# Optimization experiments

Hardware: AMD Instinct MI355X
Metric: run time of the kernel (lower is better)

## Reference

```python
import jax, jax.numpy as jnp
import numpy as np

CODEBOOK_SIZE = 1024
CODEBOOK_DIM = 64
COMMITMENT_WEIGHT = 0.25
DECAY = 0.99
EPS = 1e-5


def setup_inputs() -> dict:
    key = jax.random.key(0)
    k1, k2, k3 = jax.random.split(key, 3)
    B, D, T = 32, CODEBOOK_DIM, 4096
    z = jax.random.normal(k1, (B, D, T), dtype=jnp.float32)
    embedding = jax.random.normal(k2, (CODEBOOK_SIZE, CODEBOOK_DIM), dtype=jnp.float32)
    cluster_size = jnp.zeros((CODEBOOK_SIZE,), dtype=jnp.float32)
    embed_avg = jax.random.normal(k3, (CODEBOOK_SIZE, CODEBOOK_DIM), dtype=jnp.float32)
    return {"z": z, "embedding": embedding, "cluster_size": cluster_size, "embed_avg": embed_avg}


def reference(z, embedding, cluster_size, embed_avg):
    # z: [B, D, T]; embedding/embed_avg: [K, D]; cluster_size: [K]
    B, D, T = z.shape
    K = embedding.shape[0]
    z_flat = jnp.transpose(z, (0, 2, 1)).reshape(-1, D)  # [N, D], N = B*T

    # squared-euclidean distances via expansion (matches torch cdist expansion)
    dist = (
        jnp.sum(z_flat * z_flat, axis=1, keepdims=True)
        + jnp.sum(embedding * embedding, axis=1)
        - 2.0 * (z_flat @ embedding.T)
    )  # [N, K]
    indices = jnp.argmin(dist, axis=1)  # [N] int

    # EMA updates (training path). one_hot.sum(0) -> segment count; one_hot.T @ z_flat -> segment sum
    counts = jax.ops.segment_sum(jnp.ones(z_flat.shape[0], dtype=z_flat.dtype), indices, num_segments=K)
    new_cluster_size = cluster_size * DECAY + (1.0 - DECAY) * counts
    embed_sum = jax.ops.segment_sum(z_flat, indices, num_segments=K)  # [K, D]
    new_embed_avg = embed_avg * DECAY + (1.0 - DECAY) * embed_sum
    n = jnp.sum(new_cluster_size)
    smoothed = (new_cluster_size + EPS) / (n + K * EPS) * n  # Laplace smoothing
    new_embedding = new_embed_avg / smoothed[:, None]  # [K, D]

    # quantize with the *updated* codebook (as in the torch in-place update)
    z_q_flat = new_embedding[indices]  # [N, D] gather
    loss = COMMITMENT_WEIGHT * jnp.mean((z_flat - jax.lax.stop_gradient(z_q_flat)) ** 2)
    # straight-through estimator
    z_q_flat = z_flat + jax.lax.stop_gradient(z_q_flat - z_flat)
    z_q = jnp.transpose(z_q_flat.reshape(B, T, D), (0, 2, 1))  # [B, D, T]
    return z_q, loss, indices.reshape(B, T)
```

## Files before the change

kernel.cpp:

```cpp
#include <hip/hip_runtime.h>

#define N_PTS 131072
#define TD 4096
#define DD 64
#define KK 1024
#define MARGIN_TH 2e-3f
#define BPAD 72

typedef short bf16x8 __attribute__((ext_vector_type(8)));
typedef float f32x4  __attribute__((ext_vector_type(4)));

__device__ inline unsigned short f2bf(float f) {
    unsigned u = __float_as_uint(f);
    unsigned r = u + 0x7FFFu + ((u >> 16) & 1u);
    return (unsigned short)(r >> 16);
}
__device__ inline float bf2f(unsigned short h) {
    return __uint_as_float(((unsigned)h) << 16);
}

__global__ __launch_bounds__(256) void vq_prep(const float* __restrict__ z,
                                               unsigned short* __restrict__ zh,
                                               unsigned short* __restrict__ zl)
{
    __shared__ float tile[64][65];
    const int tid = threadIdx.x;
    const int b = blockIdx.x >> 6;
    const int t0 = (blockIdx.x & 63) * 64;

    const int d = tid >> 2, tq = tid & 3;
#pragma unroll
    for (int it = 0; it < 4; ++it) {
        const int tt = tq * 16 + it * 4;
        const float4 v = *(const float4*)(z + ((size_t)b * DD + d) * TD + t0 + tt);
        tile[d][tt] = v.x; tile[d][tt + 1] = v.y; tile[d][tt + 2] = v.z; tile[d][tt + 3] = v.w;
    }
    __syncthreads();

    const int p = tid >> 2, dg = tid & 3;
    bf16x8 h0, h1, l0, l1;
#pragma unroll
    for (int j = 0; j < 8; ++j) {
        const float v0 = tile[dg * 16 + j][p];
        const unsigned short a = f2bf(v0);
        h0[j] = (short)a; l0[j] = (short)f2bf(v0 - bf2f(a));
        const float v1 = tile[dg * 16 + 8 + j][p];
        const unsigned short c = f2bf(v1);
        h1[j] = (short)c; l1[j] = (short)f2bf(v1 - bf2f(c));
    }
    const size_t o = ((size_t)(b * TD + t0 + p)) * DD + dg * 16;
    *(bf16x8*)(zh + o) = h0;
    *(bf16x8*)(zh + o + 8) = h1;
    *(bf16x8*)(zl + o) = l0;
    *(bf16x8*)(zl + o + 8) = l1;
}

__global__ __launch_bounds__(256) void vq_eprep(const float* __restrict__ emb,
                                                unsigned short* __restrict__ eh,
                                                unsigned short* __restrict__ el,
                                                float* __restrict__ halfnorm)
{
    const int k = blockIdx.x * 256 + threadIdx.x;
    if (k >= KK) return;
    const float* e = emb + (size_t)k * DD;
    double s = 0.0;
#pragma unroll
    for (int d = 0; d < DD; ++d) {
        const float v = e[d];
        const double dv = (double)v;
        s = fma(dv, dv, s);
        const unsigned short h = f2bf(v);
        eh[(size_t)k * DD + d] = h;
        el[(size_t)k * DD + d] = f2bf(v - bf2f(h));
    }
    halfnorm[k] = (float)(0.5 * s);
}

__global__ __launch_bounds__(256, 4) void vq_screen_mfma(
    const unsigned short* __restrict__ zh, const unsigned short* __restrict__ zl,
    const unsigned short* __restrict__ eh, const unsigned short* __restrict__ el,
    const float* __restrict__ hn,
    int* __restrict__ idx_ws, float* __restrict__ ind_out,
    int* __restrict__ nflag, int* __restrict__ flags)
{
    __shared__ __align__(16) unsigned short ehs[2][16 * BPAD];
    __shared__ __align__(16) unsigned short els[2][16 * BPAD];
    __shared__ float hns[2][16];

    const int tid = threadIdx.x;
    const int lane = tid & 63;
    const int wid = tid >> 6;
    const int quad = lane >> 4;
    const int col = lane & 15;
    const int pbase = blockIdx.x * 128 + wid * 32;

    const bf16x8* pA0h = (const bf16x8*)(zh + (size_t)(pbase + col) * DD + quad * 8);
    const bf16x8* pA0l = (const bf16x8*)(zl + (size_t)(pbase + col) * DD + quad * 8);
    const bf16x8* pA1h = (const bf16x8*)(zh + (size_t)(pbase + 16 + col) * DD + quad * 8);
    const bf16x8* pA1l = (const bf16x8*)(zl + (size_t)(pbase + 16 + col) * DD + quad * 8);
    const bf16x8 A0h0 = pA0h[0], A0h1 = pA0h[4];
    const bf16x8 A0l0 = pA0l[0], A0l1 = pA0l[4];
    const bf16x8 A1h0 = pA1h[0], A1h1 = pA1h[4];
    const bf16x8 A1l0 = pA1l[0], A1l1 = pA1l[4];

    const int sidx = tid & 127;
    const int scode = sidx >> 3;
    const int schunk = sidx & 7;
    const bool shi = (tid < 128);
    const unsigned short* sgl = shi ? eh : el;
    const int soff = scode * BPAD + schunk * 8;

    {
        const bf16x8 r = *(const bf16x8*)(sgl + (size_t)scode * DD + schunk * 8);
        *(bf16x8*)((shi ? &ehs[0][0] : &els[0][0]) + soff) = r;
        if (tid < 16) hns[0][tid] = hn[tid];
    }
    __syncthreads();

    float best0[4]  = {1e30f, 1e30f, 1e30f, 1e30f};
    float best20[4] = {1e30f, 1e30f, 1e30f, 1e30f};
    int   bidx0[4]  = {0, 0, 0, 0};
    float best1[4]  = {1e30f, 1e30f, 1e30f, 1e30f};
    float best21[4] = {1e30f, 1e30f, 1e30f, 1e30f};
    int   bidx1[4]  = {0, 0, 0, 0};

    for (int t = 0; t < KK / 16; ++t) {
        const int cur = t & 1;

        bf16x8 nr;
        float nh = 0.f;
        if (t < 63) {
            nr = *(const bf16x8*)(sgl + (size_t)((t + 1) * 16 + scode) * DD + schunk * 8);
            if (tid < 16) nh = hn[(t + 1) * 16 + tid];
        }

        const unsigned short* bh = &ehs[cur][col * BPAD + quad * 8];
        const unsigned short* bl = &els[cur][col * BPAD + quad * 8];
        const bf16x8 Bh0 = *(const bf16x8*)(bh);
        const bf16x8 Bh1 = *(const bf16x8*)(bh + 32);
        const bf16x8 Bl0 = *(const bf16x8*)(bl);
        const bf16x8 Bl1 = *(const bf16x8*)(bl + 32);
        const float hnv = hns[cur][col];

        if (t < 63) {
            *(bf16x8*)((shi ? &ehs[cur ^ 1][0] : &els[cur ^ 1][0]) + soff) = nr;
            if (tid < 16) hns[cur ^ 1][tid] = nh;
        }

        f32x4 p0 = {0.f, 0.f, 0.f, 0.f}, q0 = {0.f, 0.f, 0.f, 0.f};
        f32x4 p1 = {0.f, 0.f, 0.f, 0.f}, q1 = {0.f, 0.f, 0.f, 0.f};
        p0 = __builtin_amdgcn_mfma_f32_16x16x32_bf16(A0h0, Bh0, p0, 0, 0, 0);
        p1 = __builtin_amdgcn_mfma_f32_16x16x32_bf16(A1h0, Bh0, p1, 0, 0, 0);
        q0 = __builtin_amdgcn_mfma_f32_16x16x32_bf16(A0l0, Bh0, q0, 0, 0, 0);
        q1 = __builtin_amdgcn_mfma_f32_16x16x32_bf16(A1l0, Bh0, q1, 0, 0, 0);
        p0 = __builtin_amdgcn_mfma_f32_16x16x32_bf16(A0h1, Bh1, p0, 0, 0, 0);
        p1 = __builtin_amdgcn_mfma_f32_16x16x32_bf16(A1h1, Bh1, p1, 0, 0, 0);
        q0 = __builtin_amdgcn_mfma_f32_16x16x32_bf16(A0l1, Bh1, q0, 0, 0, 0);
        q1 = __builtin_amdgcn_mfma_f32_16x16x32_bf16(A1l1, Bh1, q1, 0, 0, 0);
        p0 = __builtin_amdgcn_mfma_f32_16x16x32_bf16(A0h0, Bl0, p0, 0, 0, 0);
        p1 = __builtin_amdgcn_mfma_f32_16x16x32_bf16(A1h0, Bl0, p1, 0, 0, 0);
        q0 = __builtin_amdgcn_mfma_f32_16x16x32_bf16(A0h1, Bl1, q0, 0, 0, 0);
        q1 = __builtin_amdgcn_mfma_f32_16x16x32_bf16(A1h1, Bl1, q1, 0, 0, 0);

        const int code = t * 16 + col;
#pragma unroll
        for (int r = 0; r < 4; ++r) {
            const float s0 = hnv - (p0[r] + q0[r]);
            const bool l0 = s0 < best0[r];
            best20[r] = fminf(best20[r], fmaxf(best0[r], s0));
            best0[r] = l0 ? s0 : best0[r];
            bidx0[r] = l0 ? code : bidx0[r];
            const float s1 = hnv - (p1[r] + q1[r]);
            const bool l1 = s1 < best1[r];
            best21[r] = fminf(best21[r], fmaxf(best1[r], s1));
            best1[r] = l1 ? s1 : best1[r];
            bidx1[r] = l1 ? code : bidx1[r];
        }

        __syncthreads();
    }

#pragma unroll
    for (int off = 1; off < 16; off <<= 1) {
#pragma unroll
        for (int r = 0; r < 4; ++r) {
            {
                const float ob  = __shfl_xor(best0[r],  off, 64);
                const float ob2 = __shfl_xor(best20[r], off, 64);
                const int   oi  = __shfl_xor(bidx0[r],  off, 64);
                const float nb2 = fminf(fminf(best20[r], ob2), fmaxf(best0[r], ob));
                if (ob < best0[r]) { best0[r] = ob; bidx0[r] = oi; }
                best20[r] = nb2;
            }
            {
                const float ob  = __shfl_xor(best1[r],  off, 64);
                const float ob2 = __shfl_xor(best21[r], off, 64);
                const int   oi  = __shfl_xor(bidx1[r],  off, 64);
                const float nb2 = fminf(fminf(best21[r], ob2), fmaxf(best1[r], ob));
                if (ob < best1[r]) { best1[r] = ob; bidx1[r] = oi; }
                best21[r] = nb2;
            }
        }
    }

    if (col == 0) {
#pragma unroll
        for (int r = 0; r < 4; ++r) {
            const int n0 = pbase + quad * 4 + r;
            idx_ws[n0] = bidx0[r];
            ind_out[n0] = (float)bidx0[r];
            if (best20[r] - best0[r] < MARGIN_TH) {
                const int pos = atomicAdd(nflag, 1);
                flags[pos] = n0;
            }
            const int n1 = pbase + 16 + quad * 4 + r;
            idx_ws[n1] = bidx1[r];
            ind_out[n1] = (float)bidx1[r];
            if (best21[r] - best1[r] < MARGIN_TH) {
                const int pos = atomicAdd(nflag, 1);
                flags[pos] = n1;
            }
        }
    }
}

__global__ __launch_bounds__(256) void vq_fallback(
    const float* __restrict__ z, const float* __restrict__ emb,
    int* __restrict__ idx_ws, float* __restrict__ ind_out,
    const int* __restrict__ nflag, const int* __restrict__ flags)
{
    __shared__ float zs[4][DD];
    const int total = *nflag;
    const int lane = threadIdx.x & 63;
    const int wid = threadIdx.x >> 6;
    const int gw = blockIdx.x * 4 + wid;

    for (int i = gw; i < total; i += gridDim.x * 4) {
        const int n = flags[i];
        const int b = n >> 12, t = n & 4095;
        zs[wid][lane] = z[((size_t)b * DD + lane) * TD + t];
        __builtin_amdgcn_s_waitcnt(0);
        double best = 1e300;
        int bi = KK;
        for (int kc = 0; kc < KK / 64; ++kc) {
            const int k = kc * 64 + lane;
            const float4* e = (const float4*)(emb + (size_t)k * DD);
            double dot = 0.0, nn = 0.0;
#pragma unroll
            for (int j = 0; j < 16; ++j) {
                float4 ev = e[j];
                double e0 = (double)ev.x, e1 = (double)ev.y, e2 = (double)ev.z, e3 = (double)ev.w;
                nn = fma(e0, e0, fma(e1, e1, fma(e2, e2, fma(e3, e3, nn))));
                dot = fma((double)zs[wid][4 * j + 0], e0,
                      fma((double)zs[wid][4 * j + 1], e1,
                      fma((double)zs[wid][4 * j + 2], e2,
                      fma((double)zs[wid][4 * j + 3], e3, dot))));
            }
            double s = 0.5 * nn - dot;
            if (s < best || (s == best && k < bi)) { best = s; bi = k; }
        }
        for (int off = 32; off > 0; off >>= 1) {
            double os = __shfl_down(best, off, 64);
            int oi = __shfl_down(bi, off, 64);
            if (os < best || (os == best && oi < bi)) { best = os; bi = oi; }
        }
        if (lane == 0) { idx_ws[n] = bi; ind_out[n] = (float)bi; }
    }
}

__global__ __launch_bounds__(256) void vq_hist(const int* __restrict__ idx_ws, int* __restrict__ hist)
{
    __shared__ int h[KK];
    for (int i = threadIdx.x; i < KK; i += 256) h[i] = 0;
    __syncthreads();
    const int base = blockIdx.x * 2048;
#pragma unroll
    for (int j = 0; j < 8; ++j)
        atomicAdd(&h[idx_ws[base + j * 256 + threadIdx.x]], 1);
    __syncthreads();
    for (int i = threadIdx.x; i < KK; i += 256)
        if (h[i]) atomicAdd(&hist[i], h[i]);
}

__global__ __launch_bounds__(1024) void vq_prefix_smo(
    const int* __restrict__ hist, const float* __restrict__ cs,
    int* __restrict__ cursor, float* __restrict__ rsmo)
{
    __shared__ int tmp[KK];
    __shared__ double dred[KK];
    const int k = threadIdx.x;
    const int c = hist[k];
    tmp[k] = c;
    const double ncs = 0.99 * (double)cs[k] + 0.01 * (double)c;
    dred[k] = ncs;
    __syncthreads();
    for (int off = 1; off < KK; off <<= 1) {
        int u = (k >= off) ? tmp[k - off] : 0;
        __syncthreads();
        tmp[k] += u;
        __syncthreads();
    }
    cursor[k] = tmp[k] - c;
    for (int s = 512; s > 0; s >>= 1) {
        if (k < s) dred[k] += dred[k + s];
        __syncthreads();
    }
    const double nsum = dred[0];
    const double smo = (ncs + 1e-5) / (nsum + (double)KK * 1e-5) * nsum;
    rsmo[k] = (float)(1.0 / smo);
}

__global__ __launch_bounds__(256) void vq_scatter(const int* __restrict__ idx_ws,
                                                  int* __restrict__ cursor, int* __restrict__ order)
{
    const int n = blockIdx.x * 256 + threadIdx.x;
    const int bi = idx_ws[n];
    const int pos = atomicAdd(&cursor[bi], 1);
    order[pos] = n;
}

__global__ __launch_bounds__(256) void vq_esum2(
    const unsigned short* __restrict__ zh, const unsigned short* __restrict__ zl,
    const int* __restrict__ idx_ws, const int* __restrict__ order,
    float* __restrict__ esum)
{
    const int tid = threadIdx.x;
    const int lane = tid & 63;
    const int w = tid >> 6;
    const int base = blockIdx.x * 256 + w * 64;

    const int pid_l = order[base + lane];
    const int code_l = idx_ws[pid_l];

    float v[64];
#pragma unroll
    for (int j = 0; j < 64; ++j) {
        const int pj = __shfl(pid_l, j, 64);
        const size_t o = (size_t)pj * DD + lane;
        v[j] = bf2f(zh[o]) + bf2f(zl[o]);
    }

    float racc = 0.f;
    int cur = __shfl(code_l, 0, 64);
#pragma unroll
    for (int j = 0; j < 64; ++j) {
        const int cj = __shfl(code_l, j, 64);
        if (cj != cur) {
            atomicAdd(&esum[(size_t)cur * DD + lane], racc);
            racc = 0.f;
            cur = cj;
        }
        racc += v[j];
    }
    atomicAdd(&esum[(size_t)cur * DD + lane], racc);
}

__global__ __launch_bounds__(256) void vq_newE(
    const float* __restrict__ avg, const float* __restrict__ esum,
    const float* __restrict__ rsmo, float* __restrict__ newE)
{
    const int j = blockIdx.x * 256 + threadIdx.x;
    newE[j] = (float)((0.99 * (double)avg[j] + 0.01 * (double)esum[j]) * (double)rsmo[j >> 6]);
}

__global__ __launch_bounds__(256) void vq_gather_loss(
    const float* __restrict__ z, const float* __restrict__ newE,
    const int* __restrict__ idx_ws, float* __restrict__ zq_out,
    double* __restrict__ loss_acc, int* __restrict__ done_cnt,
    float* __restrict__ loss_out)
{
    const int tid = threadIdx.x;
    const int n = blockIdx.x * 256 + tid;
    const int b = n >> 12;
    const int t = n & 4095;
    const float* zb = z + ((size_t)b * DD) * TD + t;
    float* ob = zq_out + ((size_t)b * DD) * TD + t;
    const int bi = idx_ws[n];
    const float* e = newE + (size_t)bi * DD;
    double acc = 0.0;
#pragma unroll
    for (int d = 0; d < DD; ++d) {
        float q = e[d];
        float zv = zb[(size_t)d * TD];
        ob[(size_t)d * TD] = q;
        float df = zv - q;
        acc = fma((double)df, (double)df, acc);
    }
    for (int off = 32; off > 0; off >>= 1) acc += __shfl_down(acc, off, 64);
    __shared__ double wsum[4];
    const int wid = tid >> 6, lane = tid & 63;
    if (lane == 0) wsum[wid] = acc;
    __syncthreads();
    if (tid == 0) {
        atomicAdd(loss_acc, wsum[0] + wsum[1] + wsum[2] + wsum[3]);
        __threadfence();
        const int prev = atomicAdd(done_cnt, 1);
        if (prev == gridDim.x - 1) {
            __threadfence();
            *loss_out = (float)(0.25 * (*loss_acc) / (double)(N_PTS * DD));
        }
    }
}

extern "C" void kernel_launch(void* const* d_in, const int* in_sizes, int n_in,
                              void* d_out, int out_size, void* d_ws, size_t ws_size,
                              hipStream_t stream) {
    const float* z    = (const float*)d_in[0];
    const float* emb  = (const float*)d_in[1];
    const float* cs   = (const float*)d_in[2];
    const float* avg  = (const float*)d_in[3];

    float* out      = (float*)d_out;
    float* zq_out   = out;
    float* loss_out = out + 8388608;
    float* ind_out  = out + 8388609;

    unsigned short* zh = (unsigned short*)d_out;
    unsigned short* zl = (unsigned short*)((char*)d_out + 16777216);

    char* ws = (char*)d_ws;
    int*            idx_ws   = (int*)ws;
    float*          newE     = (float*)(ws + 524288);
    float*          esum     = (float*)(ws + 786432);
    int*            hist     = (int*)(ws + 1048576);
    int*            nflag    = (int*)(ws + 1052672);
    int*            done_cnt = (int*)(ws + 1052676);
    double*         loss_acc = (double*)(ws + 1052680);
    float*          halfnorm = (float*)(ws + 1052688);
    int*            cursor   = (int*)(ws + 1056784);
    int*            flags    = (int*)(ws + 1060880);
    int*            order    = (int*)(ws + 1585168);
    unsigned short* eh       = (unsigned short*)(ws + 2109456);
    unsigned short* el       = (unsigned short*)(ws + 2240528);
    float*          rsmo     = (float*)(ws + 2371600);

    hipMemsetAsync(ws + 786432, 0, 266256, stream);

    vq_prep<<<2048, 256, 0, stream>>>(z, zh, zl);
    vq_eprep<<<4, 256, 0, stream>>>(emb, eh, el, halfnorm);
    vq_screen_mfma<<<1024, 256, 0, stream>>>(zh, zl, eh, el, halfnorm,
                                             idx_ws, ind_out, nflag, flags);
    vq_fallback<<<128, 256, 0, stream>>>(z, emb, idx_ws, ind_out, nflag, flags);
    vq_hist<<<64, 256, 0, stream>>>(idx_ws, hist);
    vq_prefix_smo<<<1, 1024, 0, stream>>>(hist, cs, cursor, rsmo);
    vq_scatter<<<N_PTS / 256, 256, 0, stream>>>(idx_ws, cursor, order);
    vq_esum2<<<N_PTS / 256, 256, 0, stream>>>(zh, zl, idx_ws, order, esum);
    vq_newE<<<256, 256, 0, stream>>>(avg, esum, rsmo, newE);
    vq_gather_loss<<<N_PTS / 256, 256, 0, stream>>>(z, newE, idx_ws, zq_out,
                                                    loss_acc, done_cnt, loss_out);
}
```

Measured before the change: 305.3 us.

## Negate z, fold halfnorm into MFMA accumulator, direct-to-LDS codebook loads, fuse histogram

The prep kernel now stores negated z, so the MFMA accumulator can start at the half-norm and yield the distance directly, merging the p/q accumulators into one. Codebook tiles go global-to-LDS through global_load_lds with an XOR-style swizzle instead of padded register staging. Running best and second-best updates use fmed3. The separate histogram kernel is removed: the screen kernel counts with global atomics and the fallback adjusts counts when it changes an index. The risks are heavy global atomic contention on the 1024 histogram bins and sign handling in esum.

Result: slower. 332.8 us (+9.0%).

```diff
diff --git a/kernel.cpp b/kernel.cpp
--- a/kernel.cpp
+++ b/kernel.cpp
@@ -5,7 +5,6 @@
 #define DD 64
 #define KK 1024
 #define MARGIN_TH 2e-3f
-#define BPAD 72
 
 typedef short bf16x8 __attribute__((ext_vector_type(8)));
 typedef float f32x4  __attribute__((ext_vector_type(4)));
@@ -19,6 +18,12 @@
     return __uint_as_float(((unsigned)h) << 16);
 }
 
+__device__ inline void gload_lds16(const unsigned short* g, unsigned short* l) {
+    __builtin_amdgcn_global_load_lds(
+        (const __attribute__((address_space(1))) unsigned int*)g,
+        (__attribute__((address_space(3))) unsigned int*)l, 16, 0, 0);
+}
+
 __global__ __launch_bounds__(256) void vq_prep(const float* __restrict__ z,
                                                unsigned short* __restrict__ zh,
                                                unsigned short* __restrict__ zl)
@@ -41,10 +46,10 @@
     bf16x8 h0, h1, l0, l1;
 #pragma unroll
     for (int j = 0; j < 8; ++j) {
-        const float v0 = tile[dg * 16 + j][p];
+        const float v0 = -tile[dg * 16 + j][p];
         const unsigned short a = f2bf(v0);
         h0[j] = (short)a; l0[j] = (short)f2bf(v0 - bf2f(a));
-        const float v1 = tile[dg * 16 + 8 + j][p];
+        const float v1 = -tile[dg * 16 + 8 + j][p];
         const unsigned short c = f2bf(v1);
         h1[j] = (short)c; l1[j] = (short)f2bf(v1 - bf2f(c));
     }
@@ -81,18 +86,17 @@
     const unsigned short* __restrict__ eh, const unsigned short* __restrict__ el,
     const float* __restrict__ hn,
     int* __restrict__ idx_ws, float* __restrict__ ind_out,
-    int* __restrict__ nflag, int* __restrict__ flags)
-{
-    __shared__ __align__(16) unsigned short ehs[2][16 * BPAD];
-    __shared__ __align__(16) unsigned short els[2][16 * BPAD];
-    __shared__ float hns[2][16];
-
-    const int tid = threadIdx.x;
+    int* __restrict__ nflag, int* __restrict__ flags, int* __restrict__ hist)
+{
+    __shared__ __align__(16) unsigned short ehs[2][1024];
+    __shared__ __align__(16) unsigned short els[2][1024];
+
+    const int tid  = threadIdx.x;
     const int lane = tid & 63;
-    const int wid = tid >> 6;
+    const int wv   = tid >> 6;
     const int quad = lane >> 4;
-    const int col = lane & 15;
-    const int pbase = blockIdx.x * 128 + wid * 32;
+    const int col  = lane & 15;
+    const int pbase = blockIdx.x * 128 + wv * 32;
 
     const bf16x8* pA0h = (const bf16x8*)(zh + (size_t)(pbase + col) * DD + quad * 8);
     const bf16x8* pA0l = (const bf16x8*)(zl + (size_t)(pbase + col) * DD + quad * 8);
@@ -103,18 +107,19 @@
     const bf16x8 A1h0 = pA1h[0], A1h1 = pA1h[4];
     const bf16x8 A1l0 = pA1l[0], A1l1 = pA1l[4];
 
-    const int sidx = tid & 127;
-    const int scode = sidx >> 3;
-    const int schunk = sidx & 7;
-    const bool shi = (tid < 128);
-    const unsigned short* sgl = shi ? eh : el;
-    const int soff = scode * BPAD + schunk * 8;
-
-    {
-        const bf16x8 r = *(const bf16x8*)(sgl + (size_t)scode * DD + schunk * 8);
-        *(bf16x8*)((shi ? &ehs[0][0] : &els[0][0]) + soff) = r;
-        if (tid < 16) hns[0][tid] = hn[tid];
-    }
+    const int ci = tid & 127;
+    const int sc = ci >> 3, sm = ci & 7;
+    const int sj = (sm - sc) & 7;
+    const unsigned short* sgl = (tid < 128 ? eh : el) + sc * DD + sj * 8;
+    unsigned short* dst0 = (tid < 128 ? &ehs[0][0] : &els[0][0]) + (wv & 1) * 512 + lane * 8;
+    unsigned short* dst1 = dst0 + 1024;
+
+    const int pH0 = (col * 8 + ((quad + col) & 7)) * 8;
+    const int pH1 = (col * 8 + ((quad + 4 + col) & 7)) * 8;
+
+    gload_lds16(sgl, dst0);
+    float hnv_c = hn[col];
+    float hnv_n = hnv_c;
     __syncthreads();
 
     float best0[4]  = {1e30f, 1e30f, 1e30f, 1e30f};
@@ -124,60 +129,50 @@
     float best21[4] = {1e30f, 1e30f, 1e30f, 1e30f};
     int   bidx1[4]  = {0, 0, 0, 0};
 
+    int code = col;
+#pragma unroll 2
     for (int t = 0; t < KK / 16; ++t) {
         const int cur = t & 1;
-
-        bf16x8 nr;
-        float nh = 0.f;
         if (t < 63) {
-            nr = *(const bf16x8*)(sgl + (size_t)((t + 1) * 16 + scode) * DD + schunk * 8);
-            if (tid < 16) nh = hn[(t + 1) * 16 + tid];
-        }
-
-        const unsigned short* bh = &ehs[cur][col * BPAD + quad * 8];
-        const unsigned short* bl = &els[cur][col * BPAD + quad * 8];
-        const bf16x8 Bh0 = *(const bf16x8*)(bh);
-        const bf16x8 Bh1 = *(const bf16x8*)(bh + 32);
-        const bf16x8 Bl0 = *(const bf16x8*)(bl);
-        const bf16x8 Bl1 = *(const bf16x8*)(bl + 32);
-        const float hnv = hns[cur][col];
-
-        if (t < 63) {
-            *(bf16x8*)((shi ? &ehs[cur ^ 1][0] : &els[cur ^ 1][0]) + soff) = nr;
-            if (tid < 16) hns[cur ^ 1][tid] = nh;
-        }
-
-        f32x4 p0 = {0.f, 0.f, 0.f, 0.f}, q0 = {0.f, 0.f, 0.f, 0.f};
-        f32x4 p1 = {0.f, 0.f, 0.f, 0.f}, q1 = {0.f, 0.f, 0.f, 0.f};
-        p0 = __builtin_amdgcn_mfma_f32_16x16x32_bf16(A0h0, Bh0, p0, 0, 0, 0);
-        p1 = __builtin_amdgcn_mfma_f32_16x16x32_bf16(A1h0, Bh0, p1, 0, 0, 0);
-        q0 = __builtin_amdgcn_mfma_f32_16x16x32_bf16(A0l0, Bh0, q0, 0, 0, 0);
-        q1 = __builtin_amdgcn_mfma_f32_16x16x32_bf16(A1l0, Bh0, q1, 0, 0, 0);
-        p0 = __builtin_amdgcn_mfma_f32_16x16x32_bf16(A0h1, Bh1, p0, 0, 0, 0);
-        p1 = __builtin_amdgcn_mfma_f32_16x16x32_bf16(A1h1, Bh1, p1, 0, 0, 0);
-        q0 = __builtin_amdgcn_mfma_f32_16x16x32_bf16(A0l1, Bh1, q0, 0, 0, 0);
-        q1 = __builtin_amdgcn_mfma_f32_16x16x32_bf16(A1l1, Bh1, q1, 0, 0, 0);
-        p0 = __builtin_amdgcn_mfma_f32_16x16x32_bf16(A0h0, Bl0, p0, 0, 0, 0);
-        p1 = __builtin_amdgcn_mfma_f32_16x16x32_bf16(A1h0, Bl0, p1, 0, 0, 0);
-        q0 = __builtin_amdgcn_mfma_f32_16x16x32_bf16(A0h1, Bl1, q0, 0, 0, 0);
-        q1 = __builtin_amdgcn_mfma_f32_16x16x32_bf16(A1h1, Bl1, q1, 0, 0, 0);
-
-        const int code = t * 16 + col;
+            gload_lds16(sgl + (t + 1) * (16 * DD), cur ? dst0 : dst1);
+            hnv_n = hn[(t + 1) * 16 + col];
+        }
+
+        const unsigned short* bh = &ehs[cur][0];
+        const unsigned short* bl = &els[cur][0];
+        const bf16x8 Bh0 = *(const bf16x8*)(bh + pH0);
+        const bf16x8 Bh1 = *(const bf16x8*)(bh + pH1);
+        const bf16x8 Bl0 = *(const bf16x8*)(bl + pH0);
+        const bf16x8 Bl1 = *(const bf16x8*)(bl + pH1);
+
+        f32x4 a0 = {hnv_c, hnv_c, hnv_c, hnv_c};
+        f32x4 a1 = {hnv_c, hnv_c, hnv_c, hnv_c};
+        a0 = __builtin_amdgcn_mfma_f32_16x16x32_bf16(A0h0, Bh0, a0, 0, 0, 0);
+        a1 = __builtin_amdgcn_mfma_f32_16x16x32_bf16(A1h0, Bh0, a1, 0, 0, 0);
+        a0 = __builtin_amdgcn_mfma_f32_16x16x32_bf16(A0h1, Bh1, a0, 0, 0, 0);
+        a1 = __builtin_amdgcn_mfma_f32_16x16x32_bf16(A1h1, Bh1, a1, 0, 0, 0);
+        a0 = __builtin_amdgcn_mfma_f32_16x16x32_bf16(A0l0, Bh0, a0, 0, 0, 0);
+        a1 = __builtin_amdgcn_mfma_f32_16x16x32_bf16(A1l0, Bh0, a1, 0, 0, 0);
+        a0 = __builtin_amdgcn_mfma_f32_16x16x32_bf16(A0l1, Bh1, a0, 0, 0, 0);
+        a1 = __builtin_amdgcn_mfma_f32_16x16x32_bf16(A1l1, Bh1, a1, 0, 0, 0);
+        a0 = __builtin_amdgcn_mfma_f32_16x16x32_bf16(A0h0, Bl0, a0, 0, 0, 0);
+        a1 = __builtin_amdgcn_mfma_f32_16x16x32_bf16(A1h0, Bl0, a1, 0, 0, 0);
+        a0 = __builtin_amdgcn_mfma_f32_16x16x32_bf16(A0h1, Bl1, a0, 0, 0, 0);
+        a1 = __builtin_amdgcn_mfma_f32_16x16x32_bf16(A1h1, Bl1, a1, 0, 0, 0);
+
 #pragma unroll
         for (int r = 0; r < 4; ++r) {
-            const float s0 = hnv - (p0[r] + q0[r]);
-            const bool l0 = s0 < best0[r];
-            best20[r] = fminf(best20[r], fmaxf(best0[r], s0));
-            best0[r] = l0 ? s0 : best0[r];
-            bidx0[r] = l0 ? code : bidx0[r];
-            const float s1 = hnv - (p1[r] + q1[r]);
-            const bool l1 = s1 < best1[r];
-            best21[r] = fminf(best21[r], fmaxf(best1[r], s1));
-            best1[r] = l1 ? s1 : best1[r];
-            bidx1[r] = l1 ? code : bidx1[r];
+            const float s0 = a0[r];
+            best20[r] = __builtin_amdgcn_fmed3f(best0[r], best20[r], s0);
+            if (s0 < best0[r]) { best0[r] = s0; bidx0[r] = code; }
+            const float s1 = a1[r];
+            best21[r] = __builtin_amdgcn_fmed3f(best1[r], best21[r], s1);
+            if (s1 < best1[r]) { best1[r] = s1; bidx1[r] = code; }
         }
 
         __syncthreads();
+        hnv_c = hnv_n;
+        code += 16;
     }
 
 #pragma unroll
@@ -209,6 +204,7 @@
             const int n0 = pbase + quad * 4 + r;
             idx_ws[n0] = bidx0[r];
             ind_out[n0] = (float)bidx0[r];
+            atomicAdd(&hist[bidx0[r]], 1);
             if (best20[r] - best0[r] < MARGIN_TH) {
                 const int pos = atomicAdd(nflag, 1);
                 flags[pos] = n0;
@@ -216,6 +212,7 @@
             const int n1 = pbase + 16 + quad * 4 + r;
             idx_ws[n1] = bidx1[r];
             ind_out[n1] = (float)bidx1[r];
+            atomicAdd(&hist[bidx1[r]], 1);
             if (best21[r] - best1[r] < MARGIN_TH) {
                 const int pos = atomicAdd(nflag, 1);
                 flags[pos] = n1;
@@ -227,7 +224,8 @@
 __global__ __launch_bounds__(256) void vq_fallback(
     const float* __restrict__ z, const float* __restrict__ emb,
     int* __restrict__ idx_ws, float* __restrict__ ind_out,
-    const int* __restrict__ nflag, const int* __restrict__ flags)
+    const int* __restrict__ nflag, const int* __restrict__ flags,
+    int* __restrict__ hist)
 {
     __shared__ float zs[4][DD];
     const int total = *nflag;
@@ -264,22 +262,16 @@
             int oi = __shfl_down(bi, off, 64);
             if (os < best || (os == best && oi < bi)) { best = os; bi = oi; }
         }
-        if (lane == 0) { idx_ws[n] = bi; ind_out[n] = (float)bi; }
-    }
-}
-
-__global__ __launch_bounds__(256) void vq_hist(const int* __restrict__ idx_ws, int* __restrict__ hist)
-{
-    __shared__ int h[KK];
-    for (int i = threadIdx.x; i < KK; i += 256) h[i] = 0;
-    __syncthreads();
-    const int base = blockIdx.x * 2048;
-#pragma unroll
-    for (int j = 0; j < 8; ++j)
-        atomicAdd(&h[idx_ws[base + j * 256 + threadIdx.x]], 1);
-    __syncthreads();
-    for (int i = threadIdx.x; i < KK; i += 256)
-        if (h[i]) atomicAdd(&hist[i], h[i]);
+        if (lane == 0) {
+            const int old = idx_ws[n];
+            if (bi != old) {
+                idx_ws[n] = bi;
+                ind_out[n] = (float)bi;
+                atomicAdd(&hist[old], -1);
+                atomicAdd(&hist[bi], 1);
+            }
+        }
+    }
 }
 
 __global__ __launch_bounds__(1024) void vq_prefix_smo(
@@ -346,13 +338,13 @@
     for (int j = 0; j < 64; ++j) {
         const int cj = __shfl(code_l, j, 64);
         if (cj != cur) {
-            atomicAdd(&esum[(size_t)cur * DD + lane], racc);
+            atomicAdd(&esum[(size_t)cur * DD + lane], -racc);
             racc = 0.f;
             cur = cj;
         }
         racc += v[j];
     }
-    atomicAdd(&esum[(size_t)cur * DD + lane], racc);
+    atomicAdd(&esum[(size_t)cur * DD + lane], -racc);
 }
 
 __global__ __launch_bounds__(256) void vq_newE(
@@ -439,9 +431,8 @@
     vq_prep<<<2048, 256, 0, stream>>>(z, zh, zl);
     vq_eprep<<<4, 256, 0, stream>>>(emb, eh, el, halfnorm);
     vq_screen_mfma<<<1024, 256, 0, stream>>>(zh, zl, eh, el, halfnorm,
-                                             idx_ws, ind_out, nflag, flags);
-    vq_fallback<<<128, 256, 0, stream>>>(z, emb, idx_ws, ind_out, nflag, flags);
-    vq_hist<<<64, 256, 0, stream>>>(idx_ws, hist);
+                                             idx_ws, ind_out, nflag, flags, hist);
+    vq_fallback<<<128, 256, 0, stream>>>(z, emb, idx_ws, ind_out, nflag, flags, hist);
     vq_prefix_smo<<<1, 1024, 0, stream>>>(hist, cs, cursor, rsmo);
     vq_scatter<<<N_PTS / 256, 256, 0, stream>>>(idx_ws, cursor, order);
     vq_esum2<<<N_PTS / 256, 256, 0, stream>>>(zh, zl, idx_ws, order, esum);
```
